# Optimization experiments

Hardware: AMD Instinct MI355X
Metric: run time of the kernel (lower is better)

Reference implementation:

```python
import jax, jax.numpy as jnp
import numpy as np

N_HEAD = 16
N_BLOCKS = 2
EPS = 1e-6

def _rmsnorm(x, g):
    return x * jax.lax.rsqrt(jnp.mean(x * x, axis=-1, keepdims=True) + EPS) * g

def _causal_sa(x, Wqkv, Wproj, g):
    # x: (B, T, C); fused qkv, RMSNorm on q/k over full C before head split
    B, T, C = x.shape
    hd = C // N_HEAD
    q, k, v = jnp.split(x @ Wqkv, 3, axis=-1)
    q = _rmsnorm(q, g)
    k = _rmsnorm(k, g)
    def heads(t):
        return t.reshape(B, T, N_HEAD, hd).transpose(0, 2, 1, 3)
    q, k, v = heads(q), heads(k), heads(v)
    scores = jnp.einsum('bhqd,bhkd->bhqk', q, k) * (1.0 / np.sqrt(hd))
    mask = jnp.tril(jnp.ones((T, T), dtype=bool))
    scores = jnp.where(mask, scores, -jnp.finfo(scores.dtype).max)
    att = jax.nn.softmax(scores, axis=-1)
    y = jnp.einsum('bhqk,bhkd->bhqd', att, v)
    y = y.transpose(0, 2, 1, 3).reshape(B, T, C)
    return y @ Wproj

def setup_inputs() -> dict:
    key = jax.random.key(0)
    ks = jax.random.split(key, 8)
    B, ng, T, C = 2, 8, 256, 1024
    M_loc, M_glob = 16, 16
    s = 0.02
    return {
        'x': jax.random.normal(ks[0], (B, ng, T, C), jnp.float32),
        'mem_tokens': jax.random.normal(ks[1], (B, M_glob, C), jnp.float32),
        'local_mem': jax.random.normal(ks[2], (B, ng, M_loc, C), jnp.float32),
        'Wqkv_loc': jax.random.normal(ks[3], (N_BLOCKS, C, 3 * C), jnp.float32) * s,
        'Wproj_loc': jax.random.normal(ks[4], (N_BLOCKS, C, C), jnp.float32) * s,
        'g_loc': jnp.ones((N_BLOCKS, C), jnp.float32),
        'Wqkv_glob': jax.random.normal(ks[5], (N_BLOCKS, C, 3 * C), jnp.float32) * s,
        'Wproj_glob': jax.random.normal(ks[6], (N_BLOCKS, C, C), jnp.float32) * s,
        'g_glob': jnp.ones((N_BLOCKS, C), jnp.float32),
    }

def reference(x, mem_tokens, local_mem, Wqkv_loc, Wproj_loc, g_loc, Wqkv_glob, Wproj_glob, g_glob):
    B, ng, T, C = x.shape
    M_loc = local_mem.shape[2]
    M_glob = mem_tokens.shape[1]
    for i in range(N_BLOCKS):
        # local causal SA: per-group, with local mem tokens prepended
        xl = jnp.concatenate([local_mem, x], axis=2).reshape(B * ng, M_loc + T, C)
        yl = _causal_sa(xl, Wqkv_loc[i], Wproj_loc[i], g_loc[i])
        yl = yl.reshape(B, ng, M_loc + T, C)
        local_mem = yl[:, :, :M_loc, :]
        x = yl[:, :, M_loc:, :]
        # global causal SA over flattened sequence with global mem tokens
        xg = x.reshape(B, ng * T, C)
        xg = jnp.concatenate([mem_tokens, xg], axis=1)
        yg = _causal_sa(xg, Wqkv_glob[i], Wproj_glob[i], g_glob[i])
        mem_tokens = yg[:, :M_glob, :]
        x = yg[:, M_glob:, :].reshape(B, ng, T, C)
    return x
```

## Files before the change

kernel.cpp:

```cpp
#include <hip/hip_runtime.h>
#include <hip/hip_bf16.h>
#include <math.h>

typedef __attribute__((ext_vector_type(8))) short s16x8;
typedef __attribute__((ext_vector_type(4))) short s16x4;
typedef __attribute__((ext_vector_type(4))) float f32x4;

#define MPAD 4352
#define LG 2064
#define CT 8
#define SM_SHIFT 11.5415603f

__device__ __forceinline__ short f2b(float f) {
  unsigned u = __float_as_uint(f);
  unsigned r = (u + 0x7fffu + ((u >> 16) & 1u)) >> 16;
  return (short)(unsigned short)r;
}
__device__ __forceinline__ float b2f(short s) {
  return __uint_as_float(((unsigned)(unsigned short)s) << 16);
}
__device__ __forceinline__ float fexp2(float x) {
#if __has_builtin(__builtin_amdgcn_exp2f)
  return __builtin_amdgcn_exp2f(x);
#else
  float r;
  asm("v_exp_f32 %0, %1" : "=v"(r) : "v"(x));
  return r;
#endif
}
__device__ __forceinline__ int cvtpk(float lo, float hi) {
  int r;
  asm("v_cvt_pk_bf16_f32 %0, %1, %2" : "=v"(r) : "v"(lo), "v"(hi));
  return r;
}

__device__ __forceinline__ void gl_lds16(const short* g, short* l) {
  __builtin_amdgcn_global_load_lds((const __attribute__((address_space(1))) short*)g,
                                   (__attribute__((address_space(3))) short*)l, 16, 0, 0);
}

__global__ __launch_bounds__(256) void transpose_cast(const float* __restrict__ in,
                                                      short* __restrict__ out,
                                                      int K, int N) {
  __shared__ float tile[32][33];
  int bn = blockIdx.x * 32;
  int bk = blockIdx.y * 32;
  for (int i = threadIdx.y; i < 32; i += 8)
    tile[i][threadIdx.x] = in[(size_t)(bk + i) * N + bn + threadIdx.x];
  __syncthreads();
  for (int i = threadIdx.y; i < 32; i += 8)
    out[(size_t)(bn + i) * K + bk + threadIdx.x] = f2b(tile[threadIdx.x][i]);
}

__global__ __launch_bounds__(256) void transpose_v(const short* __restrict__ QKV,
                                                   short* __restrict__ Vt,
                                                   int L, int Lpad) {
  __shared__ short tile[32][33];
  int sh = blockIdx.z;
  int s = sh >> 4, h = sh & 15;
  int kb = blockIdx.x * 32;
  int cb = blockIdx.y * 32;
  int tx = threadIdx.x;
  for (int i = threadIdx.y; i < 32; i += 8) {
    int key = kb + i;
    if (key > L - 1) key = L - 1;
    tile[i][tx] = QKV[(size_t)(s * L + key) * 3072 + 2048 + h * 64 + cb + tx];
  }
  __syncthreads();
  for (int i = threadIdx.y; i < 32; i += 8)
    Vt[((size_t)sh * 64 + cb + i) * Lpad + kb + tx] = tile[tx][i];
}

__global__ __launch_bounds__(256) void gemm_bt3(const short* __restrict__ A,
                                                const short* __restrict__ BT,
                                                short* __restrict__ C,
                                                int K, int N) {
  __shared__ short As[2][128 * 32];
  __shared__ short Bs[2][128 * 32];
  const int tid = threadIdx.x;
  const int lane = tid & 63;
  const int w = tid >> 6;
  const int wr = (w >> 1) * 64, wc = (w & 1) * 64;
  const int m0 = blockIdx.y * 128;
  const int n0 = blockIdx.x * 128;
  const int l15 = lane & 15, lhi = lane >> 4;

  f32x4 acc[4][4] = {};

  auto STAGE = [&](int b, int k0) {
#pragma unroll
    for (int p = 0; p < 2; ++p) {
      int g = w * 128 + p * 64 + lane;
      int row = g >> 2;
      int cs = (g & 3) * 8;
      gl_lds16(A + (size_t)(m0 + row) * K + k0 + cs, &As[b][g * 8]);
      gl_lds16(BT + (size_t)(n0 + row) * K + k0 + cs, &Bs[b][g * 8]);
    }
  };

  const int nt = K >> 5;
  STAGE(0, 0);
  __syncthreads();
  int cur = 0;
  for (int t = 0; t < nt; ++t) {
    if (t + 1 < nt) STAGE(cur ^ 1, (t + 1) << 5);
    s16x8 af[4], bf[4];
#pragma unroll
    for (int m = 0; m < 4; ++m)
      af[m] = *(const s16x8*)(&As[cur][(wr + m * 16 + l15) * 32 + lhi * 8]);
#pragma unroll
    for (int n = 0; n < 4; ++n)
      bf[n] = *(const s16x8*)(&Bs[cur][(wc + n * 16 + l15) * 32 + lhi * 8]);
#pragma unroll
    for (int m = 0; m < 4; ++m)
#pragma unroll
      for (int n = 0; n < 4; ++n)
        acc[m][n] = __builtin_amdgcn_mfma_f32_16x16x32_bf16(af[m], bf[n], acc[m][n], 0, 0, 0);
    __syncthreads();
    cur ^= 1;
  }
#pragma unroll
  for (int m = 0; m < 4; ++m) {
    int row_base = m0 + wr + m * 16 + lhi * 4;
#pragma unroll
    for (int n = 0; n < 4; ++n) {
      int col = n0 + wc + n * 16 + l15;
#pragma unroll
      for (int r = 0; r < 4; ++r)
        C[(size_t)(row_base + r) * N + col] = f2b(acc[m][n][r]);
    }
  }
}

__global__ __launch_bounds__(256) void rmsnorm_qk(short* __restrict__ QKV,
                                                  const float* __restrict__ g) {
  int row = blockIdx.x;
  int which = blockIdx.y;
  size_t base = (size_t)row * 3072 + (size_t)which * 1024;
  int t = threadIdx.x;
  s16x4 in = *(const s16x4*)(QKV + base + t * 4);
  float v[4];
  float ss = 0.f;
#pragma unroll
  for (int j = 0; j < 4; ++j) {
    v[j] = b2f(in[j]);
    ss += v[j] * v[j];
  }
#pragma unroll
  for (int m = 32; m >= 1; m >>= 1) ss += __shfl_xor(ss, m);
  __shared__ float red[4];
  if ((t & 63) == 0) red[t >> 6] = ss;
  __syncthreads();
  float tot = red[0] + red[1] + red[2] + red[3];
  float inv = rsqrtf(tot * (1.0f / 1024.0f) + 1e-6f);
  if (which == 0) inv *= 0.125f * 1.44269504f;
  s16x4 out;
#pragma unroll
  for (int j = 0; j < 4; ++j) out[j] = f2b(v[j] * inv * g[t * 4 + j]);
  *(s16x4*)(&QKV[base + t * 4]) = out;
}


__global__ __launch_bounds__(256) void attn_causal4(const short* __restrict__ QKV,
                                                    const short* __restrict__ Vt,
                                                    short* __restrict__ Y,
                                                    int L, int Lpad) {
  const int h = blockIdx.y, s = blockIdx.z;
  const int q0 = blockIdx.x * 64;
  const int tid = threadIdx.x;
  const int lane = tid & 63, w = tid >> 6;
  const int l15 = lane & 15, lhi = lane >> 4;
  const int row0 = s * L;

  __shared__ short Ks[2][64][72];
  __shared__ short Vs[2][64][72];

  int qld = q0 + w * 16 + l15;
  if (qld > L - 1) qld = L - 1;
  const size_t qrow = (size_t)(row0 + qld) * 3072 + h * 64;
  s16x8 qf0 = *(const s16x8*)(QKV + qrow + lhi * 8);
  s16x8 qf1 = *(const s16x8*)(QKV + qrow + 32 + lhi * 8);

  float lsum = 0.f;
  f32x4 o[4];
#pragma unroll
  for (int d = 0; d < 4; ++d) o[d] = f32x4{0.f, 0.f, 0.f, 0.f};

  const short* Vbase = Vt + (size_t)(s * 16 + h) * 64 * Lpad;
  const int sA = (lhi & 1) * 32 + l15;
  const int sB = sA + 16;
  const int bh = lhi >> 1;

  s16x8 kreg[2], vreg[2];
#pragma unroll
  for (int p = 0; p < 2; ++p) {
    int g = tid + p * 256;
    int kr = g >> 3, cs = (g & 7) * 8;
    int krow = kr;
    if (krow > L - 1) krow = L - 1;
    kreg[p] = *(const s16x8*)(QKV + (size_t)(row0 + krow) * 3072 + 1024 + h * 64 + cs);
    vreg[p] = *(const s16x8*)(Vbase + (size_t)kr * Lpad + cs);
  }

  int buf = 0;
  for (int kb = 0; kb <= q0; kb += 64, buf ^= 1) {
#pragma unroll
    for (int p = 0; p < 2; ++p) {
      int g = tid + p * 256;
      int kr = g >> 3, cs = (g & 7) * 8;
      *(s16x8*)(&Ks[buf][kr][cs]) = kreg[p];
      *(s16x8*)(&Vs[buf][kr][cs]) = vreg[p];
    }
    __syncthreads();
    if (kb + 64 <= q0) {
#pragma unroll
      for (int p = 0; p < 2; ++p) {
        int g = tid + p * 256;
        int kr = g >> 3, cs = (g & 7) * 8;
        int krow = kb + 64 + kr;
        if (krow > L - 1) krow = L - 1;
        kreg[p] = *(const s16x8*)(QKV + (size_t)(row0 + krow) * 3072 + 1024 + h * 64 + cs);
        vreg[p] = *(const s16x8*)(Vbase + (size_t)kr * Lpad + kb + 64 + cs);
      }
    }

    f32x4 st[4];
#pragma unroll
    for (int n = 0; n < 4; ++n) {
      s16x8 k0 = *(const s16x8*)(&Ks[buf][n * 16 + l15][lhi * 8]);
      s16x8 k1 = *(const s16x8*)(&Ks[buf][n * 16 + l15][32 + lhi * 8]);
      f32x4 sa = f32x4{-SM_SHIFT, -SM_SHIFT, -SM_SHIFT, -SM_SHIFT};
      sa = __builtin_amdgcn_mfma_f32_16x16x32_bf16(k0, qf0, sa, 0, 0, 0);
      sa = __builtin_amdgcn_mfma_f32_16x16x32_bf16(k1, qf1, sa, 0, 0, 0);
      st[n] = sa;
    }

    if (kb == q0) {
      int q = q0 + w * 16 + l15;
#pragma unroll
      for (int n = 0; n < 4; ++n) {
#pragma unroll
        for (int r = 0; r < 4; ++r) {
          int key = kb + n * 16 + lhi * 4 + r;
          if (key > q) st[n][r] = -1e30f;
        }
      }
    }

    int wd[4][2];
#pragma unroll
    for (int n = 0; n < 4; ++n) {
      float p0 = fexp2(st[n][0]), p1 = fexp2(st[n][1]);
      float p2 = fexp2(st[n][2]), p3 = fexp2(st[n][3]);
      lsum += (p0 + p1) + (p2 + p3);
      wd[n][0] = cvtpk(p0, p1);
      wd[n][1] = cvtpk(p2, p3);
    }

#pragma unroll
    for (int kk = 0; kk < 2; ++kk) {
      int a0 = __shfl(wd[2 * kk][0], sA), a1 = __shfl(wd[2 * kk][1], sA);
      int a2 = __shfl(wd[2 * kk][0], sB), a3 = __shfl(wd[2 * kk][1], sB);
      int b0 = __shfl(wd[2 * kk + 1][0], sA), b1 = __shfl(wd[2 * kk + 1][1], sA);
      int b2 = __shfl(wd[2 * kk + 1][0], sB), b3 = __shfl(wd[2 * kk + 1][1], sB);
      int pw[4];
      pw[0] = bh ? b0 : a0;
      pw[1] = bh ? b1 : a1;
      pw[2] = bh ? b2 : a2;
      pw[3] = bh ? b3 : a3;
      s16x8 pa = *(const s16x8*)pw;
#pragma unroll
      for (int d = 0; d < 4; ++d) {
        s16x8 vf = *(const s16x8*)(&Vs[buf][d * 16 + l15][kk * 32 + lhi * 8]);
        o[d] = __builtin_amdgcn_mfma_f32_16x16x32_bf16(pa, vf, o[d], 0, 0, 0);
      }
    }
  }

  lsum += __shfl_xor(lsum, 16);
  lsum += __shfl_xor(lsum, 32);
  float lsq[4];
#pragma unroll
  for (int r = 0; r < 4; ++r) lsq[r] = __shfl(lsum, lhi * 4 + r);
#pragma unroll
  for (int d = 0; d < 4; ++d) {
#pragma unroll
    for (int r = 0; r < 4; ++r) {
      int qr = q0 + w * 16 + lhi * 4 + r;
      if (qr < L)
        Y[(size_t)(row0 + qr) * 1024 + h * 64 + d * 16 + l15] = f2b(o[d][r] / lsq[r]);
    }
  }
}

__global__ __launch_bounds__(256) void attn_split2(const short* __restrict__ QKV,
                                                   const short* __restrict__ Vt,
                                                   float* __restrict__ o_acc,
                                                   float* __restrict__ ls_acc) {
  const int qb = blockIdx.x;
  const int chunk = blockIdx.y;
  const int sh = blockIdx.z;
  const int t0 = chunk * CT;
  if (t0 > qb) return;
  const int t1 = min(t0 + CT, qb + 1);
  const int h = sh & 15, s = sh >> 4;
  const int q0 = qb * 64;
  const int tid = threadIdx.x;
  const int lane = tid & 63, w = tid >> 6;
  const int l15 = lane & 15, lhi = lane >> 4;
  const int row0 = s * LG;
  const int Lpad = 2112;

  __shared__ short Ks[2][64][72];
  __shared__ short Vs[2][64][72];

  int qld = q0 + w * 16 + l15;
  if (qld > LG - 1) qld = LG - 1;
  const size_t qrow = (size_t)(row0 + qld) * 3072 + h * 64;
  s16x8 qf0 = *(const s16x8*)(QKV + qrow + lhi * 8);
  s16x8 qf1 = *(const s16x8*)(QKV + qrow + 32 + lhi * 8);

  float lsum = 0.f;
  f32x4 o[4];
#pragma unroll
  for (int d = 0; d < 4; ++d) o[d] = f32x4{0.f, 0.f, 0.f, 0.f};

  const short* Vbase = Vt + (size_t)sh * 64 * Lpad;
  const int sA = (lhi & 1) * 32 + l15;
  const int sB = sA + 16;
  const int bh = lhi >> 1;

  s16x8 kreg[2], vreg[2];
  const int kb0 = t0 * 64;
#pragma unroll
  for (int p = 0; p < 2; ++p) {
    int g = tid + p * 256;
    int kr = g >> 3, cs = (g & 7) * 8;
    int krow = kb0 + kr;
    if (krow > LG - 1) krow = LG - 1;
    kreg[p] = *(const s16x8*)(QKV + (size_t)(row0 + krow) * 3072 + 1024 + h * 64 + cs);
    vreg[p] = *(const s16x8*)(Vbase + (size_t)kr * Lpad + kb0 + cs);
  }

  int buf = 0;
  for (int t = t0; t < t1; ++t, buf ^= 1) {
    const int kb = t * 64;
#pragma unroll
    for (int p = 0; p < 2; ++p) {
      int g = tid + p * 256;
      int kr = g >> 3, cs = (g & 7) * 8;
      *(s16x8*)(&Ks[buf][kr][cs]) = kreg[p];
      *(s16x8*)(&Vs[buf][kr][cs]) = vreg[p];
    }
    __syncthreads();
    if (t + 1 < t1) {
#pragma unroll
      for (int p = 0; p < 2; ++p) {
        int g = tid + p * 256;
        int kr = g >> 3, cs = (g & 7) * 8;
        int krow = kb + 64 + kr;
        if (krow > LG - 1) krow = LG - 1;
        kreg[p] = *(const s16x8*)(QKV + (size_t)(row0 + krow) * 3072 + 1024 + h * 64 + cs);
        vreg[p] = *(const s16x8*)(Vbase + (size_t)kr * Lpad + kb + 64 + cs);
      }
    }

    f32x4 st[4];
#pragma unroll
    for (int n = 0; n < 4; ++n) {
      s16x8 k0 = *(const s16x8*)(&Ks[buf][n * 16 + l15][lhi * 8]);
      s16x8 k1 = *(const s16x8*)(&Ks[buf][n * 16 + l15][32 + lhi * 8]);
      f32x4 sa = f32x4{-SM_SHIFT, -SM_SHIFT, -SM_SHIFT, -SM_SHIFT};
      sa = __builtin_amdgcn_mfma_f32_16x16x32_bf16(k0, qf0, sa, 0, 0, 0);
      sa = __builtin_amdgcn_mfma_f32_16x16x32_bf16(k1, qf1, sa, 0, 0, 0);
      st[n] = sa;
    }

    if (t == qb) {
      int q = q0 + w * 16 + l15;
#pragma unroll
      for (int n = 0; n < 4; ++n) {
#pragma unroll
        for (int r = 0; r < 4; ++r) {
          int key = kb + n * 16 + lhi * 4 + r;
          if (key > q) st[n][r] = -1e30f;
        }
      }
    }

    int wd[4][2];
#pragma unroll
    for (int n = 0; n < 4; ++n) {
      float p0 = fexp2(st[n][0]), p1 = fexp2(st[n][1]);
      float p2 = fexp2(st[n][2]), p3 = fexp2(st[n][3]);
      lsum += (p0 + p1) + (p2 + p3);
      wd[n][0] = cvtpk(p0, p1);
      wd[n][1] = cvtpk(p2, p3);
    }

#pragma unroll
    for (int kk = 0; kk < 2; ++kk) {
      int a0 = __shfl(wd[2 * kk][0], sA), a1 = __shfl(wd[2 * kk][1], sA);
      int a2 = __shfl(wd[2 * kk][0], sB), a3 = __shfl(wd[2 * kk][1], sB);
      int b0 = __shfl(wd[2 * kk + 1][0], sA), b1 = __shfl(wd[2 * kk + 1][1], sA);
      int b2 = __shfl(wd[2 * kk + 1][0], sB), b3 = __shfl(wd[2 * kk + 1][1], sB);
      int pw[4];
      pw[0] = bh ? b0 : a0;
      pw[1] = bh ? b1 : a1;
      pw[2] = bh ? b2 : a2;
      pw[3] = bh ? b3 : a3;
      s16x8 pa = *(const s16x8*)pw;
#pragma unroll
      for (int d = 0; d < 4; ++d) {
        s16x8 vf = *(const s16x8*)(&Vs[buf][d * 16 + l15][kk * 32 + lhi * 8]);
        o[d] = __builtin_amdgcn_mfma_f32_16x16x32_bf16(pa, vf, o[d], 0, 0, 0);
      }
    }
  }

  lsum += __shfl_xor(lsum, 16);
  lsum += __shfl_xor(lsum, 32);
  int qmy = q0 + w * 16 + l15;
  if (lhi == 0 && qmy < LG) atomicAdd(&ls_acc[(size_t)sh * LG + qmy], lsum);
#pragma unroll
  for (int r = 0; r < 4; ++r) {
    int qr = q0 + w * 16 + lhi * 4 + r;
    if (qr < LG) {
#pragma unroll
      for (int d = 0; d < 4; ++d)
        atomicAdd(&o_acc[((size_t)sh * LG + qr) * 64 + d * 16 + l15], o[d][r]);
    }
  }
}

__global__ __launch_bounds__(256) void attn_merge(const float* __restrict__ o_acc,
                                                  const float* __restrict__ ls_acc,
                                                  short* __restrict__ Y) {
  int sh = blockIdx.z * 16 + blockIdx.y;
  int s = sh >> 4, h = sh & 15;
  int row = blockIdx.x * 4 + (threadIdx.x >> 6);
  int col = threadIdx.x & 63;
  if (row < LG) {
    float inv = 1.0f / ls_acc[(size_t)sh * LG + row];
    float v = o_acc[((size_t)sh * LG + row) * 64 + col];
    Y[(size_t)(s * LG + row) * 1024 + h * 64 + col] = f2b(v * inv);
  }
}

__global__ __launch_bounds__(256) void build_xl(const float* __restrict__ x,
                                                const float* __restrict__ lm,
                                                short* __restrict__ Xin) {
  int row = blockIdx.x;
  int s = row / 272, r = row % 272;
  const float* src = (r < 16) ? lm + ((size_t)s * 16 + r) * 1024
                              : x + ((size_t)s * 256 + (r - 16)) * 1024;
  int t = threadIdx.x;
  f32x4 v = *(const f32x4*)(src + t * 4);
  s16x4 o;
#pragma unroll
  for (int j = 0; j < 4; ++j) o[j] = f2b(v[j]);
  *(s16x4*)(&Xin[(size_t)row * 1024 + t * 4]) = o;
}

__global__ __launch_bounds__(256) void split_local_build_xg(const short* __restrict__ Pout,
                                                            const float* __restrict__ mem_src,
                                                            float* __restrict__ lm_out,
                                                            short* __restrict__ Xin) {
  int row = blockIdx.x;
  int t = threadIdx.x;
  if (row < 4352) {
    int sr = row < 4128 ? row : 4127;
    int b = sr / 2064, r = sr % 2064;
    s16x4 o;
    if (r < 16) {
      f32x4 v = *(const f32x4*)(mem_src + ((size_t)(b * 16 + r)) * 1024 + t * 4);
#pragma unroll
      for (int j = 0; j < 4; ++j) o[j] = f2b(v[j]);
    } else {
      int f = b * 2048 + (r - 16);
      int pr = (f >> 8) * 272 + 16 + (f & 255);
      o = *(const s16x4*)(Pout + (size_t)pr * 1024 + t * 4);
    }
    *(s16x4*)(&Xin[(size_t)row * 1024 + t * 4]) = o;
  } else {
    int m = row - 4352;
    int pr = (m >> 4) * 272 + (m & 15);
    s16x4 v = *(const s16x4*)(Pout + (size_t)pr * 1024 + t * 4);
    f32x4 o;
#pragma unroll
    for (int j = 0; j < 4; ++j) o[j] = b2f(v[j]);
    *(f32x4*)(&lm_out[(size_t)m * 1024 + t * 4]) = o;
  }
}

__global__ __launch_bounds__(256) void split_global_build_xl(const short* __restrict__ Pout,
                                                             const float* __restrict__ lm_src,
                                                             float* __restrict__ mem_out,
                                                             short* __restrict__ Xin) {
  int row = blockIdx.x;
  int t = threadIdx.x;
  if (row < 4352) {
    int s = row / 272, r = row % 272;
    s16x4 o;
    if (r < 16) {
      f32x4 v = *(const f32x4*)(lm_src + ((size_t)(s * 16 + r)) * 1024 + t * 4);
#pragma unroll
      for (int j = 0; j < 4; ++j) o[j] = f2b(v[j]);
    } else {
      int f = s * 256 + (r - 16);
      int pr = (f >> 11) * 2064 + 16 + (f & 2047);
      o = *(const s16x4*)(Pout + (size_t)pr * 1024 + t * 4);
    }
    *(s16x4*)(&Xin[(size_t)row * 1024 + t * 4]) = o;
  } else {
    int m = row - 4352;
    int pr = (m >> 4) * 2064 + (m & 15);
    s16x4 v = *(const s16x4*)(Pout + (size_t)pr * 1024 + t * 4);
    f32x4 o;
#pragma unroll
    for (int j = 0; j < 4; ++j) o[j] = b2f(v[j]);
    *(f32x4*)(&mem_out[(size_t)m * 1024 + t * 4]) = o;
  }
}

__global__ __launch_bounds__(256) void split_global_final(const short* __restrict__ Pout,
                                                          float* __restrict__ out) {
  int f = blockIdx.x;
  int t = threadIdx.x;
  int pr = (f >> 11) * 2064 + 16 + (f & 2047);
  s16x4 v = *(const s16x4*)(Pout + (size_t)pr * 1024 + t * 4);
  f32x4 o;
#pragma unroll
  for (int j = 0; j < 4; ++j) o[j] = b2f(v[j]);
  *(f32x4*)(&out[(size_t)f * 1024 + t * 4]) = o;
}

extern "C" void kernel_launch(void* const* d_in, const int* in_sizes, int n_in,
                              void* d_out, int out_size, void* d_ws, size_t ws_size,
                              hipStream_t stream) {
  const float* x_in = (const float*)d_in[0];
  const float* mem_in = (const float*)d_in[1];
  const float* lm_in = (const float*)d_in[2];
  const float* Wqkv_loc = (const float*)d_in[3];
  const float* Wproj_loc = (const float*)d_in[4];
  const float* g_loc = (const float*)d_in[5];
  const float* Wqkv_glob = (const float*)d_in[6];
  const float* Wproj_glob = (const float*)d_in[7];
  const float* g_glob = (const float*)d_in[8];

  char* ws = (char*)d_ws;
  size_t off = 0;
  auto alloc = [&](size_t bytes) {
    char* p = ws + off;
    off += (bytes + 255) & ~(size_t)255;
    return p;
  };
  short* Wt = (short*)alloc((size_t)3072 * 1024 * 2);
  float* lm_cur = (float*)alloc((size_t)256 * 1024 * 4);
  float* mem_cur = (float*)alloc((size_t)32 * 1024 * 4);
  short* Xin = (short*)alloc((size_t)MPAD * 1024 * 2);
  short* QKVb = (short*)alloc((size_t)MPAD * 3072 * 2);
  short* Yb = (short*)alloc((size_t)MPAD * 1024 * 2);
  short* Pout = (short*)alloc((size_t)MPAD * 1024 * 2);
  short* Vtb = (short*)alloc((size_t)256 * 64 * 320 * 2);
  size_t oacc_bytes = (size_t)32 * LG * 64 * 4;
  size_t lacc_bytes = (size_t)32 * LG * 4;
  float* o_acc = (float*)alloc(oacc_bytes);
  float* ls_acc = (float*)alloc(lacc_bytes);
  const bool use_split = (ws_size >= off);

  for (int i = 0; i < 2; ++i) {
    transpose_cast<<<dim3(96, 32), dim3(32, 8), 0, stream>>>(
        Wqkv_loc + (size_t)i * 1024 * 3072, Wt, 1024, 3072);
    if (i == 0) build_xl<<<4352, 256, 0, stream>>>(x_in, lm_in, Xin);
    gemm_bt3<<<dim3(24, 34), 256, 0, stream>>>(Xin, Wt, QKVb, 1024, 3072);
    rmsnorm_qk<<<dim3(4352, 2), 256, 0, stream>>>(QKVb, g_loc + (size_t)i * 1024);
    transpose_v<<<dim3(10, 2, 256), dim3(32, 8), 0, stream>>>(QKVb, Vtb, 272, 320);
    attn_causal4<<<dim3(5, 16, 16), 256, 0, stream>>>(QKVb, Vtb, Yb, 272, 320);
    transpose_cast<<<dim3(32, 32), dim3(32, 8), 0, stream>>>(
        Wproj_loc + (size_t)i * 1024 * 1024, Wt, 1024, 1024);
    gemm_bt3<<<dim3(8, 34), 256, 0, stream>>>(Yb, Wt, Pout, 1024, 1024);
    split_local_build_xg<<<4608, 256, 0, stream>>>(Pout, i == 0 ? mem_in : mem_cur,
                                                   lm_cur, Xin);

    transpose_cast<<<dim3(96, 32), dim3(32, 8), 0, stream>>>(
        Wqkv_glob + (size_t)i * 1024 * 3072, Wt, 1024, 3072);
    gemm_bt3<<<dim3(24, 34), 256, 0, stream>>>(Xin, Wt, QKVb, 1024, 3072);
    rmsnorm_qk<<<dim3(4128, 2), 256, 0, stream>>>(QKVb, g_glob + (size_t)i * 1024);
    transpose_v<<<dim3(66, 2, 32), dim3(32, 8), 0, stream>>>(QKVb, Vtb, 2064, 2112);
    if (use_split) {
      hipMemsetAsync(o_acc, 0, oacc_bytes, stream);
      hipMemsetAsync(ls_acc, 0, lacc_bytes, stream);
      attn_split2<<<dim3(33, 5, 32), 256, 0, stream>>>(QKVb, Vtb, o_acc, ls_acc);
      attn_merge<<<dim3(516, 16, 2), 256, 0, stream>>>(o_acc, ls_acc, Yb);
    } else {
      attn_causal4<<<dim3(33, 16, 2), 256, 0, stream>>>(QKVb, Vtb, Yb, 2064, 2112);
    }
    transpose_cast<<<dim3(32, 32), dim3(32, 8), 0, stream>>>(
        Wproj_glob + (size_t)i * 1024 * 1024, Wt, 1024, 1024);
    gemm_bt3<<<dim3(8, 34), 256, 0, stream>>>(Yb, Wt, Pout, 1024, 1024);
    if (i == 0)
      split_global_build_xl<<<4384, 256, 0, stream>>>(Pout, lm_cur, mem_cur, Xin);
    else
      split_global_final<<<4096, 256, 0, stream>>>(Pout, (float*)d_out);
  }
}
```

Before: 590.2 us.

## Add 256x256-tile 8-wave phased GEMM for QKV projections

```diff
diff --git a/kernel.cpp b/kernel.cpp
--- a/kernel.cpp
+++ b/kernel.cpp
@@ -71,6 +71,149 @@
     Vt[((size_t)sh * 64 + cb + i) * Lpad + kb + tx] = tile[tx][i];
 }
 
+#define QROW(MI, AX)                                                                  \
+  acc[MI][0] = __builtin_amdgcn_mfma_f32_16x16x32_bf16(AX, b0, acc[MI][0], 0, 0, 0);  \
+  acc[MI][1] = __builtin_amdgcn_mfma_f32_16x16x32_bf16(AX, b1, acc[MI][1], 0, 0, 0);  \
+  acc[MI][2] = __builtin_amdgcn_mfma_f32_16x16x32_bf16(AX, b2, acc[MI][2], 0, 0, 0);  \
+  acc[MI][3] = __builtin_amdgcn_mfma_f32_16x16x32_bf16(AX, b3, acc[MI][3], 0, 0, 0);
+
+#define RD12(B, S)                                                              \
+  a0 = rdA(B, S, 0); a1 = rdA(B, S, 1); a2 = rdA(B, S, 2); a3 = rdA(B, S, 3);   \
+  a4 = rdA(B, S, 4); a5 = rdA(B, S, 5); a6 = rdA(B, S, 6); a7 = rdA(B, S, 7);   \
+  b0 = rdB(B, S, 0); b1 = rdB(B, S, 1); b2 = rdB(B, S, 2); b3 = rdB(B, S, 3);
+
+__global__ __launch_bounds__(512, 2) void gemm_8ph(const short* __restrict__ A,
+                                                   const short* __restrict__ BT,
+                                                   short* __restrict__ C,
+                                                   int K, int N) {
+  extern __shared__ short lds[];
+  short* Asb = lds;
+  short* Bsb = lds + 32768;
+  const int tid = threadIdx.x;
+  const int lane = tid & 63, wid = tid >> 6;
+  const int wm = wid >> 2, wn = wid & 3;
+  const int l15 = lane & 15, lhi = lane >> 4;
+  const int m0 = blockIdx.y * 256;
+  const int n0 = blockIdx.x * 256;
+
+  f32x4 acc[8][4] = {};
+
+  auto stageA = [&](int b, int h, int kt) {
+#pragma unroll
+    for (int j = 0; j < 2; ++j) {
+      int u = j * 512 + tid;
+      int row = u >> 3, slot = u & 7;
+      int ss = slot ^ (row & 7);
+      gl_lds16(A + (size_t)(m0 + h * 128 + row) * K + kt * 64 + ss * 8,
+               Asb + (b * 2 + h) * 8192 + u * 8);
+    }
+  };
+  auto stageB = [&](int b, int h, int kt) {
+#pragma unroll
+    for (int j = 0; j < 2; ++j) {
+      int u = j * 512 + tid;
+      int row = u >> 3, slot = u & 7;
+      int ss = slot ^ (row & 7);
+      gl_lds16(BT + (size_t)(n0 + h * 128 + row) * K + kt * 64 + ss * 8,
+               Bsb + (b * 2 + h) * 8192 + u * 8);
+    }
+  };
+  auto rdA = [&](int b, int s, int mf) -> s16x8 {
+    int row = mf * 16 + l15;
+    int sl = ((s << 2) | lhi) ^ (row & 7);
+    return *(const s16x8*)(Asb + (b * 2 + wm) * 8192 + row * 64 + sl * 8);
+  };
+  auto rdB = [&](int b, int s, int nf) -> s16x8 {
+    int row = (wn & 1) * 64 + nf * 16 + l15;
+    int sl = ((s << 2) | lhi) ^ (row & 7);
+    return *(const s16x8*)(Bsb + (b * 2 + (wn >> 1)) * 8192 + row * 64 + sl * 8);
+  };
+
+  const int NT = K >> 7;
+
+  stageA(0, 0, 0); stageA(0, 1, 0); stageB(0, 0, 0); stageB(0, 1, 0);
+  stageA(1, 0, 1); stageA(1, 1, 1);
+  asm volatile("s_waitcnt vmcnt(4)" ::: "memory");
+  __builtin_amdgcn_s_barrier();
+
+  s16x8 a0, a1, a2, a3, a4, a5, a6, a7, b0, b1, b2, b3;
+
+  for (int t = 0; t < NT; ++t) {
+    const bool last = (t == NT - 1);
+    const int kt1 = 2 * t + 1;
+    RD12(0, 0)
+    stageB(1, 0, kt1);
+    __builtin_amdgcn_s_barrier();
+    __builtin_amdgcn_s_setprio(1);
+    QROW(0, a0) QROW(1, a1) QROW(2, a2) QROW(3, a3)
+    __builtin_amdgcn_s_setprio(0);
+    __builtin_amdgcn_s_barrier();
+    stageB(1, 1, kt1);
+    __builtin_amdgcn_s_barrier();
+    __builtin_amdgcn_s_setprio(1);
+    QROW(4, a4) QROW(5, a5) QROW(6, a6) QROW(7, a7)
+    __builtin_amdgcn_s_setprio(0);
+    __builtin_amdgcn_s_barrier();
+    RD12(0, 1)
+    __builtin_amdgcn_s_barrier();
+    __builtin_amdgcn_s_setprio(1);
+    QROW(0, a0) QROW(1, a1) QROW(2, a2) QROW(3, a3)
+    __builtin_amdgcn_s_setprio(0);
+    __builtin_amdgcn_s_barrier();
+    if (!last) {
+      stageA(0, 0, 2 * t + 2); stageA(0, 1, 2 * t + 2);
+      asm volatile("s_waitcnt vmcnt(4)" ::: "memory");
+    } else {
+      asm volatile("s_waitcnt vmcnt(0)" ::: "memory");
+    }
+    __builtin_amdgcn_s_barrier();
+    __builtin_amdgcn_s_setprio(1);
+    QROW(4, a4) QROW(5, a5) QROW(6, a6) QROW(7, a7)
+    __builtin_amdgcn_s_setprio(0);
+    __builtin_amdgcn_s_barrier();
+    RD12(1, 0)
+    if (!last) stageB(0, 0, 2 * t + 2);
+    __builtin_amdgcn_s_barrier();
+    __builtin_amdgcn_s_setprio(1);
+    QROW(0, a0) QROW(1, a1) QROW(2, a2) QROW(3, a3)
+    __builtin_amdgcn_s_setprio(0);
+    __builtin_amdgcn_s_barrier();
+    if (!last) stageB(0, 1, 2 * t + 2);
+    __builtin_amdgcn_s_barrier();
+    __builtin_amdgcn_s_setprio(1);
+    QROW(4, a4) QROW(5, a5) QROW(6, a6) QROW(7, a7)
+    __builtin_amdgcn_s_setprio(0);
+    __builtin_amdgcn_s_barrier();
+    RD12(1, 1)
+    __builtin_amdgcn_s_barrier();
+    __builtin_amdgcn_s_setprio(1);
+    QROW(0, a0) QROW(1, a1) QROW(2, a2) QROW(3, a3)
+    __builtin_amdgcn_s_setprio(0);
+    __builtin_amdgcn_s_barrier();
+    if (!last) {
+      stageA(1, 0, kt1 + 2); stageA(1, 1, kt1 + 2);
+      asm volatile("s_waitcnt vmcnt(4)" ::: "memory");
+    }
+    __builtin_amdgcn_s_barrier();
+    __builtin_amdgcn_s_setprio(1);
+    QROW(4, a4) QROW(5, a5) QROW(6, a6) QROW(7, a7)
+    __builtin_amdgcn_s_setprio(0);
+    __builtin_amdgcn_s_barrier();
+  }
+
+#pragma unroll
+  for (int mf = 0; mf < 8; ++mf) {
+    int row_base = m0 + wm * 128 + mf * 16 + lhi * 4;
+#pragma unroll
+    for (int nf = 0; nf < 4; ++nf) {
+      int col = n0 + wn * 64 + nf * 16 + l15;
+#pragma unroll
+      for (int r = 0; r < 4; ++r)
+        C[(size_t)(row_base + r) * N + col] = f2b(acc[mf][nf][r]);
+    }
+  }
+}
+
 __global__ __launch_bounds__(256) void gemm_bt3(const short* __restrict__ A,
                                                 const short* __restrict__ BT,
                                                 short* __restrict__ C,
@@ -160,7 +303,6 @@
   *(s16x4*)(&QKV[base + t * 4]) = out;
 }
 
-
 __global__ __launch_bounds__(256) void attn_causal4(const short* __restrict__ QKV,
                                                     const short* __restrict__ Vt,
                                                     short* __restrict__ Y,
@@ -261,13 +403,13 @@
     for (int kk = 0; kk < 2; ++kk) {
       int a0 = __shfl(wd[2 * kk][0], sA), a1 = __shfl(wd[2 * kk][1], sA);
       int a2 = __shfl(wd[2 * kk][0], sB), a3 = __shfl(wd[2 * kk][1], sB);
-      int b0 = __shfl(wd[2 * kk + 1][0], sA), b1 = __shfl(wd[2 * kk + 1][1], sA);
-      int b2 = __shfl(wd[2 * kk + 1][0], sB), b3 = __shfl(wd[2 * kk + 1][1], sB);
+      int c0 = __shfl(wd[2 * kk + 1][0], sA), c1 = __shfl(wd[2 * kk + 1][1], sA);
+      int c2 = __shfl(wd[2 * kk + 1][0], sB), c3 = __shfl(wd[2 * kk + 1][1], sB);
       int pw[4];
-      pw[0] = bh ? b0 : a0;
-      pw[1] = bh ? b1 : a1;
-      pw[2] = bh ? b2 : a2;
-      pw[3] = bh ? b3 : a3;
+      pw[0] = bh ? c0 : a0;
+      pw[1] = bh ? c1 : a1;
+      pw[2] = bh ? c2 : a2;
+      pw[3] = bh ? c3 : a3;
       s16x8 pa = *(const s16x8*)pw;
 #pragma unroll
       for (int d = 0; d < 4; ++d) {
@@ -402,13 +544,13 @@
     for (int kk = 0; kk < 2; ++kk) {
       int a0 = __shfl(wd[2 * kk][0], sA), a1 = __shfl(wd[2 * kk][1], sA);
       int a2 = __shfl(wd[2 * kk][0], sB), a3 = __shfl(wd[2 * kk][1], sB);
-      int b0 = __shfl(wd[2 * kk + 1][0], sA), b1 = __shfl(wd[2 * kk + 1][1], sA);
-      int b2 = __shfl(wd[2 * kk + 1][0], sB), b3 = __shfl(wd[2 * kk + 1][1], sB);
+      int c0 = __shfl(wd[2 * kk + 1][0], sA), c1 = __shfl(wd[2 * kk + 1][1], sA);
+      int c2 = __shfl(wd[2 * kk + 1][0], sB), c3 = __shfl(wd[2 * kk + 1][1], sB);
       int pw[4];
-      pw[0] = bh ? b0 : a0;
-      pw[1] = bh ? b1 : a1;
-      pw[2] = bh ? b2 : a2;
-      pw[3] = bh ? b3 : a3;
+      pw[0] = bh ? c0 : a0;
+      pw[1] = bh ? c1 : a1;
+      pw[2] = bh ? c2 : a2;
+      pw[3] = bh ? c3 : a3;
       s16x8 pa = *(const s16x8*)pw;
 #pragma unroll
       for (int d = 0; d < 4; ++d) {
@@ -547,6 +689,13 @@
   const float* Wqkv_glob = (const float*)d_in[6];
   const float* Wproj_glob = (const float*)d_in[7];
   const float* g_glob = (const float*)d_in[8];
+
+  static bool attr_set = false;
+  if (!attr_set) {
+    hipFuncSetAttribute((const void*)gemm_8ph,
+                        hipFuncAttributeMaxDynamicSharedMemorySize, 131072);
+    attr_set = true;
+  }
 
   char* ws = (char*)d_ws;
   size_t off = 0;
@@ -573,7 +722,7 @@
     transpose_cast<<<dim3(96, 32), dim3(32, 8), 0, stream>>>(
         Wqkv_loc + (size_t)i * 1024 * 3072, Wt, 1024, 3072);
     if (i == 0) build_xl<<<4352, 256, 0, stream>>>(x_in, lm_in, Xin);
-    gemm_bt3<<<dim3(24, 34), 256, 0, stream>>>(Xin, Wt, QKVb, 1024, 3072);
+    gemm_8ph<<<dim3(12, 17), 512, 131072, stream>>>(Xin, Wt, QKVb, 1024, 3072);
     rmsnorm_qk<<<dim3(4352, 2), 256, 0, stream>>>(QKVb, g_loc + (size_t)i * 1024);
     transpose_v<<<dim3(10, 2, 256), dim3(32, 8), 0, stream>>>(QKVb, Vtb, 272, 320);
     attn_causal4<<<dim3(5, 16, 16), 256, 0, stream>>>(QKVb, Vtb, Yb, 272, 320);
@@ -585,7 +734,7 @@
 
     transpose_cast<<<dim3(96, 32), dim3(32, 8), 0, stream>>>(
         Wqkv_glob + (size_t)i * 1024 * 3072, Wt, 1024, 3072);
-    gemm_bt3<<<dim3(24, 34), 256, 0, stream>>>(Xin, Wt, QKVb, 1024, 3072);
+    gemm_8ph<<<dim3(12, 17), 512, 131072, stream>>>(Xin, Wt, QKVb, 1024, 3072);
     rmsnorm_qk<<<dim3(4128, 2), 256, 0, stream>>>(QKVb, g_glob + (size_t)i * 1024);
     transpose_v<<<dim3(66, 2, 32), dim3(32, 8), 0, stream>>>(QKVb, Vtb, 2064, 2112);
     if (use_split) {
```

Result: faster. 529.6 us (-10.3%).
